# Performance work log

Hardware: AMD Instinct MI355X
Metric: run time of the kernel (lower is better)

## Reference

```python
import jax, jax.numpy as jnp
import numpy as np

F = 128
E = 100000   # num_edges
T = 1000000  # num_triplets


def setup_inputs() -> dict:
    key = jax.random.key(0)
    ks = jax.random.split(key, 20)
    s = 0.05
    return {
        "f": jax.random.normal(ks[0], (E, 2 * F), jnp.float32),
        "M01": jax.random.normal(ks[1], (T, F), jnp.float32),
        "M02": jax.random.normal(ks[2], (T, F), jnp.float32),
        # split_net MLP([2F, 2F, 2F]): Linear -> act -> Linear
        "W1": jax.random.normal(ks[3], (2 * F, 2 * F), jnp.float32) * s,
        "b1": jnp.zeros((2 * F,), jnp.float32),
        "W2": jax.random.normal(ks[4], (2 * F, 2 * F), jnp.float32) * s,
        "b2": jnp.zeros((2 * F,), jnp.float32),
        "Ws01": jax.random.normal(ks[5], (F, F), jnp.float32) * s,
        "bs01": jnp.zeros((F,), jnp.float32),
        "Ws02": jax.random.normal(ks[6], (F, F), jnp.float32) * s,
        "bs02": jnp.zeros((F,), jnp.float32),
        "Ws": jax.random.normal(ks[7], (2 * F, F), jnp.float32) * s,
        "bs": jnp.zeros((F,), jnp.float32),
        "Wout": jax.random.normal(ks[8], (F, F), jnp.float32) * s,
        "bout": jnp.zeros((F,), jnp.float32),
        "num_edges": E,
        "idx_ji": jax.random.randint(ks[9], (T,), 0, E, jnp.int32),
        "idx_ki": jax.random.randint(ks[10], (T,), 0, E, jnp.int32),
    }


def reference(f, M01, M02, W1, b1, W2, b2, Ws01, bs01, Ws02, bs02, Ws, bs,
              Wout, bout, num_edges, idx_ji, idx_ki):
    act = jax.nn.silu
    # f = act(split_net(f)); split_net = Linear -> act -> Linear
    h = act(act(f @ W1 + b1) @ W2 + b2)          # [E, 2F]
    f01, f02 = jnp.split(h, 2, axis=-1)           # [E, F] each
    # triplet interaction: gather -> multiply -> linear -> act
    s01 = act((f01[idx_ki] * M01 * f01[idx_ji]) @ Ws01 + bs01)  # [T, F]
    s02 = act((f02[idx_ki] * M02 * f02[idx_ji]) @ Ws02 + bs02)  # [T, F]
    s = act(jnp.concatenate((s01, s02), axis=-1) @ Ws + bs)     # [T, F]
    # scatter-sum triplets back to edges
    out = jax.ops.segment_sum(s, idx_ji, num_segments=num_edges)  # [E, F]
    return out @ Wout + bout
```

## Files before the change

kernel.cpp:

```cpp
#include <hip/hip_runtime.h>

typedef __attribute__((ext_vector_type(8))) short short8;
typedef __attribute__((ext_vector_type(4))) float f32x4;

__device__ __forceinline__ float silu_f(float x) { return x / (1.0f + __expf(-x)); }

__device__ __forceinline__ unsigned short f2bf(float x) {
  unsigned u = __float_as_uint(x);
  u += 0x7FFFu + ((u >> 16) & 1u);
  return (unsigned short)(u >> 16);
}
__device__ __forceinline__ float bf2f(unsigned short v) {
  return __uint_as_float(((unsigned)v) << 16);
}
__device__ __forceinline__ unsigned cvtpk_bf16(float lo, float hi) {
  unsigned r;
  asm("v_cvt_pk_bf16_f32 %0, %1, %2" : "=v"(r) : "v"(lo), "v"(hi));
  return r;
}

#define TSYNC() do { asm volatile("s_waitcnt lgkmcnt(0)" ::: "memory"); \
                     __builtin_amdgcn_s_barrier(); \
                     asm volatile("" ::: "memory"); } while (0)

__device__ __forceinline__ void prep_one(const float* __restrict__ W,
                                         unsigned short* __restrict__ wh,
                                         unsigned short* __restrict__ wl,
                                         int N, int e)
{
  int k = e / N, n = e % N;
  float w = W[e];
  unsigned short hi = f2bf(w);
  unsigned short lo = f2bf(w - bf2f(hi));
  int kp = k >> 6, kk = k & 63;
  size_t dst = (size_t)kp * N * 64 + (size_t)n * 64 + ((((kk >> 3) ^ (n & 7)) << 3)) + (kk & 7);
  wh[dst] = hi;
  wl[dst] = lo;
}

__global__ void prep_all(const float* __restrict__ W1, unsigned short* w1h, unsigned short* w1l,
                         const float* __restrict__ W2, unsigned short* w2h, unsigned short* w2l,
                         const float* __restrict__ Wo, unsigned short* woh, unsigned short* wol)
{
  int e = blockIdx.x * 256 + threadIdx.x;
  if (e < 256 * 256) {
    prep_one(W1, w1h, w1l, 256, e);
    prep_one(W2, w2h, w2l, 256, e);
  }
  if (e < 128 * 128) prep_one(Wo, woh, wol, 128, e);
}

template<int INBF, int ASPLIT>
__global__ __launch_bounds__(512)
void mlp_gemm(const void* A_, const unsigned short* __restrict__ wh,
              const unsigned short* __restrict__ wl,
              const float* __restrict__ bias, unsigned short* __restrict__ C, int M)
{
  __shared__ unsigned short aTh[64 * 64], aTl[64 * 64];
  __shared__ unsigned short whb[256 * 64], wlb[256 * 64];
  const int tid = threadIdx.x;
  const int lane = tid & 63, wv = tid >> 6;
  const int g = wv & 3, hh = wv >> 2;
  const int l15 = lane & 15, l4 = lane >> 4;
  const int row0 = blockIdx.x * 64;
  const int r = tid >> 3, kseg = (tid & 7) * 8;
  const f32x4 zero4 = {0.f, 0.f, 0.f, 0.f};

  f32x4 acc[8];
#pragma unroll
  for (int nt = 0; nt < 8; nt++) acc[nt] = zero4;

  for (int kp = 0; kp < 4; kp++) {
    {
      const int grow = row0 + r;
      float x[8];
      if (grow < M) {
        if (INBF) {
          short8 v = *(const short8*)((const unsigned short*)A_ + (size_t)grow * 256 + kp * 64 + kseg);
#pragma unroll
          for (int j = 0; j < 8; j++) x[j] = bf2f((unsigned short)v[j]);
        } else {
          const float* ap = (const float*)A_ + (size_t)grow * 256 + kp * 64 + kseg;
          float4 v0 = *(const float4*)ap;
          float4 v1 = *(const float4*)(ap + 4);
          x[0] = v0.x; x[1] = v0.y; x[2] = v0.z; x[3] = v0.w;
          x[4] = v1.x; x[5] = v1.y; x[6] = v1.z; x[7] = v1.w;
        }
      } else {
#pragma unroll
        for (int j = 0; j < 8; j++) x[j] = 0.f;
      }
      union { short8 s; unsigned short us[8]; } H, L;
#pragma unroll
      for (int j = 0; j < 8; j++) {
        H.us[j] = f2bf(x[j]);
        L.us[j] = ASPLIT ? f2bf(x[j] - bf2f(H.us[j])) : (unsigned short)0;
      }
      const int dst = r * 64 + ((((kseg >> 3) ^ (r & 7)) << 3));
      *(short8*)(aTh + dst) = H.s;
      if (ASPLIT) *(short8*)(aTl + dst) = L.s;
    }
    {
      const short8* srcH = (const short8*)(wh + (size_t)kp * 16384);
      const short8* srcL = (const short8*)(wl + (size_t)kp * 16384);
#pragma unroll
      for (int i = 0; i < 4; i++) {
        ((short8*)whb)[tid + 512 * i] = srcH[tid + 512 * i];
        ((short8*)wlb)[tid + 512 * i] = srcL[tid + 512 * i];
      }
    }
    __syncthreads();
#pragma unroll
    for (int ks = 0; ks < 2; ks++) {
      const int arow = 16 * g + l15;
      const int aof = arow * 64 + (((4 * ks + l4) ^ (arow & 7)) << 3);
      short8 ah = *(const short8*)(aTh + aof);
      short8 al = *(const short8*)(aTl + aof);
#pragma unroll
      for (int nt = 0; nt < 8; nt++) {
        const int col = 128 * hh + 16 * nt + l15;
        const int bof = col * 64 + (((4 * ks + l4) ^ (col & 7)) << 3);
        short8 bh = *(const short8*)(whb + bof);
        short8 bl = *(const short8*)(wlb + bof);
        acc[nt] = __builtin_amdgcn_mfma_f32_16x16x32_bf16(ah, bh, acc[nt], 0, 0, 0);
        acc[nt] = __builtin_amdgcn_mfma_f32_16x16x32_bf16(ah, bl, acc[nt], 0, 0, 0);
        if (ASPLIT)
          acc[nt] = __builtin_amdgcn_mfma_f32_16x16x32_bf16(al, bh, acc[nt], 0, 0, 0);
      }
    }
    __syncthreads();
  }
#pragma unroll
  for (int nt = 0; nt < 8; nt++) {
    const int col = 128 * hh + 16 * nt + l15;
    const float bv = bias[col];
#pragma unroll
    for (int i = 0; i < 4; i++) {
      const int row = row0 + 16 * g + 4 * l4 + i;
      if (row < M) C[(size_t)row * 256 + col] = f2bf(silu_f(acc[nt][i] + bv));
    }
  }
}

__global__ __launch_bounds__(512)
void final_gemm(const float* __restrict__ A, const unsigned short* __restrict__ wh,
                const unsigned short* __restrict__ wl,
                const float* __restrict__ bias, float* __restrict__ C, int M)
{
  __shared__ unsigned short aTh[64 * 64], aTl[64 * 64];
  __shared__ unsigned short whb[128 * 64], wlb[128 * 64];
  const int tid = threadIdx.x;
  const int lane = tid & 63, wv = tid >> 6;
  const int g = wv & 3, hh = wv >> 2;
  const int l15 = lane & 15, l4 = lane >> 4;
  const int row0 = blockIdx.x * 64;
  const int r = tid >> 3, kseg = (tid & 7) * 8;
  const f32x4 zero4 = {0.f, 0.f, 0.f, 0.f};

  f32x4 acc[4];
#pragma unroll
  for (int nt = 0; nt < 4; nt++) acc[nt] = zero4;

  for (int kp = 0; kp < 2; kp++) {
    {
      const int grow = row0 + r;
      float x[8];
      if (grow < M) {
        const float* ap = A + (size_t)grow * 128 + kp * 64 + kseg;
        float4 v0 = *(const float4*)ap;
        float4 v1 = *(const float4*)(ap + 4);
        x[0] = v0.x; x[1] = v0.y; x[2] = v0.z; x[3] = v0.w;
        x[4] = v1.x; x[5] = v1.y; x[6] = v1.z; x[7] = v1.w;
      } else {
#pragma unroll
        for (int j = 0; j < 8; j++) x[j] = 0.f;
      }
      union { short8 s; unsigned short us[8]; } H, L;
#pragma unroll
      for (int j = 0; j < 8; j++) {
        H.us[j] = f2bf(x[j]);
        L.us[j] = f2bf(x[j] - bf2f(H.us[j]));
      }
      const int dst = r * 64 + ((((kseg >> 3) ^ (r & 7)) << 3));
      *(short8*)(aTh + dst) = H.s;
      *(short8*)(aTl + dst) = L.s;
    }
    {
      const short8* srcH = (const short8*)(wh + (size_t)kp * 8192);
      const short8* srcL = (const short8*)(wl + (size_t)kp * 8192);
#pragma unroll
      for (int i = 0; i < 2; i++) {
        ((short8*)whb)[tid + 512 * i] = srcH[tid + 512 * i];
        ((short8*)wlb)[tid + 512 * i] = srcL[tid + 512 * i];
      }
    }
    __syncthreads();
#pragma unroll
    for (int ks = 0; ks < 2; ks++) {
      const int arow = 16 * g + l15;
      const int aof = arow * 64 + (((4 * ks + l4) ^ (arow & 7)) << 3);
      short8 ah = *(const short8*)(aTh + aof);
      short8 al = *(const short8*)(aTl + aof);
#pragma unroll
      for (int nt = 0; nt < 4; nt++) {
        const int col = 64 * hh + 16 * nt + l15;
        const int bof = col * 64 + (((4 * ks + l4) ^ (col & 7)) << 3);
        short8 bh = *(const short8*)(whb + bof);
        short8 bl = *(const short8*)(wlb + bof);
        acc[nt] = __builtin_amdgcn_mfma_f32_16x16x32_bf16(ah, bh, acc[nt], 0, 0, 0);
        acc[nt] = __builtin_amdgcn_mfma_f32_16x16x32_bf16(ah, bl, acc[nt], 0, 0, 0);
        acc[nt] = __builtin_amdgcn_mfma_f32_16x16x32_bf16(al, bh, acc[nt], 0, 0, 0);
      }
    }
    __syncthreads();
  }
#pragma unroll
  for (int nt = 0; nt < 4; nt++) {
    const int col = 64 * hh + 16 * nt + l15;
    const float bv = bias[col];
#pragma unroll
    for (int i = 0; i < 4; i++) {
      const int row = row0 + 16 * g + 4 * l4 + i;
      if (row < M) C[(size_t)row * 128 + col] = acc[nt][i] + bv;
    }
  }
}

__global__ void hist_k(const int* __restrict__ ji, int* __restrict__ cnt, int T) {
  int t = blockIdx.x * 256 + threadIdx.x;
  const int stride = gridDim.x * 256;
  for (; t < T; t += stride) atomicAdd(&cnt[ji[t]], 1);
}

__global__ void scan1_k(const int* __restrict__ cnt, int* __restrict__ csum, int E) {
  __shared__ int red[256];
  const int c0 = blockIdx.x * 2048;
  int s = 0;
  for (int i = threadIdx.x; i < 2048; i += 256) {
    int e = c0 + i;
    if (e < E) s += cnt[e];
  }
  red[threadIdx.x] = s;
  __syncthreads();
  for (int o = 128; o > 0; o >>= 1) {
    if (threadIdx.x < o) red[threadIdx.x] += red[threadIdx.x + o];
    __syncthreads();
  }
  if (threadIdx.x == 0) csum[blockIdx.x] = red[0];
}

__global__ void scan2_k(int* __restrict__ csum, int n) {
  if (threadIdx.x == 0 && blockIdx.x == 0) {
    int acc = 0;
    for (int i = 0; i < n; i++) { int v = csum[i]; csum[i] = acc; acc += v; }
  }
}

__global__ void scan3_k(const int* __restrict__ cnt, const int* __restrict__ csum,
                        int* __restrict__ off, int E) {
  __shared__ int ts[256];
  const int c0 = blockIdx.x * 2048;
  const int tid = threadIdx.x;
  int loc[8];
  int s = 0;
#pragma unroll
  for (int k = 0; k < 8; k++) {
    int e = c0 + tid * 8 + k;
    loc[k] = (e < E) ? cnt[e] : 0;
    s += loc[k];
  }
  ts[tid] = s;
  __syncthreads();
  for (int o = 1; o < 256; o <<= 1) {
    int v = (tid >= o) ? ts[tid - o] : 0;
    __syncthreads();
    ts[tid] += v;
    __syncthreads();
  }
  int base = csum[blockIdx.x] + ((tid > 0) ? ts[tid - 1] : 0);
#pragma unroll
  for (int k = 0; k < 8; k++) {
    int e = c0 + tid * 8 + k;
    if (e < E) { off[e] = base; base += loc[k]; }
  }
}

__global__ void scatter_k(const int* __restrict__ ji, int* __restrict__ cursor,
                          int* __restrict__ perm, int T) {
  int t = blockIdx.x * 256 + threadIdx.x;
  const int stride = gridDim.x * 256;
  for (; t < T; t += stride) {
    int e = ji[t];
    int p = atomicAdd(&cursor[e], 1);
    perm[p] = t;
  }
}

struct G12 {
  short8 a0, a1;
  short8 b0, b1;
  float4 m0, m1, m2, m3;
};

__device__ __forceinline__ void issue12(G12& g, const unsigned short* __restrict__ fa,
                                        const unsigned short* __restrict__ fb,
                                        const float* __restrict__ mm, int cseg)
{
  g.a0 = *(const short8*)(fa + cseg);
  g.a1 = *(const short8*)(fa + cseg + 8);
  g.b0 = *(const short8*)(fb + cseg);
  g.b1 = *(const short8*)(fb + cseg + 8);
  g.m0 = *(const float4*)(mm + cseg + 0);
  g.m1 = *(const float4*)(mm + cseg + 4);
  g.m2 = *(const float4*)(mm + cseg + 8);
  g.m3 = *(const float4*)(mm + cseg + 12);
}

__device__ __forceinline__ void pack8x(const short8& a, const short8& b,
                                       const float4& m0, const float4& m1, short8& o)
{
  float p[8];
  p[0] = bf2f((unsigned short)a[0]) * m0.x * bf2f((unsigned short)b[0]);
  p[1] = bf2f((unsigned short)a[1]) * m0.y * bf2f((unsigned short)b[1]);
  p[2] = bf2f((unsigned short)a[2]) * m0.z * bf2f((unsigned short)b[2]);
  p[3] = bf2f((unsigned short)a[3]) * m0.w * bf2f((unsigned short)b[3]);
  p[4] = bf2f((unsigned short)a[4]) * m1.x * bf2f((unsigned short)b[4]);
  p[5] = bf2f((unsigned short)a[5]) * m1.y * bf2f((unsigned short)b[5]);
  p[6] = bf2f((unsigned short)a[6]) * m1.z * bf2f((unsigned short)b[6]);
  p[7] = bf2f((unsigned short)a[7]) * m1.w * bf2f((unsigned short)b[7]);
  union { short8 s; unsigned u[4]; } t;
  t.u[0] = cvtpk_bf16(p[0], p[1]);
  t.u[1] = cvtpk_bf16(p[2], p[3]);
  t.u[2] = cvtpk_bf16(p[4], p[5]);
  t.u[3] = cvtpk_bf16(p[6], p[7]);
  o = t.s;
}

__device__ __forceinline__ void pack16(const G12& g, short8& lo, short8& hi)
{
  pack8x(g.a0, g.b0, g.m0, g.m1, lo);
  pack8x(g.a1, g.b1, g.m2, g.m3, hi);
}

__device__ __forceinline__ void writep(unsigned short* pb, int r, int cseg,
                                       const short8& lo, const short8& hi)
{
  const int c0 = cseg >> 3;
  *(short8*)(pb + r * 128 + (((c0) ^ (r & 7)) << 3)) = lo;
  *(short8*)(pb + r * 128 + (((c0 + 1) ^ (r & 7)) << 3)) = hi;
}

__device__ __forceinline__ void mfma_block4(const unsigned short* abuf,
                                            const unsigned short* wF,
                                            f32x4 (&acc)[4],
                                            int g, int hh, int lane, int l15, int l4)
{
  const int arow = 16 * g + l15;
  __builtin_amdgcn_s_setprio(1);
#pragma unroll
  for (int ks = 0; ks < 4; ks++) {
    short8 a = *(const short8*)(abuf + arow * 128 + (((4 * ks + l4) ^ (arow & 7)) << 3));
#pragma unroll
    for (int ct = 0; ct < 4; ct++) {
      const short8 b = *(const short8*)(wF + (((4 * hh + ct) * 4 + ks) * 64 + lane) * 8);
      acc[ct] = __builtin_amdgcn_mfma_f32_16x16x32_bf16(a, b, acc[ct], 0, 0, 0);
    }
  }
  __builtin_amdgcn_s_setprio(0);
}

__device__ __forceinline__ void store_s(unsigned short* pbuf, const f32x4 (&acc)[4],
                                        const float* __restrict__ bias,
                                        int g, int hh, int l15, int l4)
{
#pragma unroll
  for (int ct = 0; ct < 4; ct++) {
    const int col = 64 * hh + 16 * ct + l15;
    const float bv = bias[col];
#pragma unroll
    for (int i = 0; i < 4; i++) {
      const int r = 16 * g + 4 * l4 + i;
      float v = silu_f(acc[ct][i] + bv);
      pbuf[r * 128 + ((((col >> 3) ^ (r & 7)) << 3)) + (col & 7)] = f2bf(v);
    }
  }
}

__global__ __launch_bounds__(512, 2)
void triplet_fused(const unsigned short* __restrict__ h,
                   const float* __restrict__ M01, const float* __restrict__ M02,
                   const float* __restrict__ Ws01, const float* __restrict__ bs01,
                   const float* __restrict__ Ws02, const float* __restrict__ bs02,
                   const float* __restrict__ Ws,   const float* __restrict__ bs,
                   const int* __restrict__ idx_ji, const int* __restrict__ idx_ki,
                   const int* __restrict__ perm,
                   float* __restrict__ out_acc, int T)
{
  __shared__ unsigned short wF01[16384];
  __shared__ unsigned short wF02[16384];
  __shared__ unsigned short wFA[16384];
  __shared__ unsigned short wFB[16384];
  __shared__ unsigned short pbA[64 * 128];
  __shared__ unsigned short pbB[64 * 128];

  const int tid = threadIdx.x;

  for (int e = tid; e < 16384; e += 512) {
    const int j = e & 7, ln = (e >> 3) & 63, ks = (e >> 9) & 3, ct = e >> 11;
    const int col = 16 * ct + (ln & 15);
    const int k = 32 * ks + 8 * (ln >> 4) + j;
    const int src = k * 128 + col;
    wF01[e] = f2bf(Ws01[src]);
    wF02[e] = f2bf(Ws02[src]);
    wFA[e]  = f2bf(Ws[src]);
    wFB[e]  = f2bf(Ws[16384 + src]);
  }
  __syncthreads();

  const int lane = tid & 63;
  const int wv = tid >> 6;
  const int g = wv & 3;
  const int hh = wv >> 2;
  const int l15 = lane & 15, l4 = lane >> 4;
  const f32x4 zero4 = {0.f, 0.f, 0.f, 0.f};

  float bsv[4];
#pragma unroll
  for (int ct = 0; ct < 4; ct++) bsv[ct] = bs[64 * hh + 16 * ct + l15];

  const int r = tid >> 3;
  const int cseg = (tid & 7) * 16;
  const int ntiles = T >> 6;
  const int G = gridDim.x;

  int tile = blockIdx.x;
  if (tile >= ntiles) return;

  auto srow = [&](int q) { int s = q * 64 + r; return s < T ? s : T - 1; };

  int trow1, trow2, trow3;
  int ek1, ej1, ek2, ej2;
  {
    const int trow0 = perm[srow(tile)];
    trow1 = perm[srow(tile + G)];
    trow2 = perm[srow(tile + 2 * G)];
    const int ek0 = idx_ki[trow0], ej0 = idx_ji[trow0];
    ek1 = idx_ki[trow1]; ej1 = idx_ji[trow1];
    ek2 = idx_ki[trow2]; ej2 = idx_ji[trow2];

    G12 gP;
    issue12(gP, h + (size_t)ek0 * 256, h + (size_t)ej0 * 256, M01 + (size_t)trow0 * 128, cseg);
    trow3 = trow0;
    (void)gP;
    short8 tmplo, tmphi;
    (void)tmplo; (void)tmphi;
  }

  G12 gA, gB, g2;
  short8 p01lo, p01hi;
  {
    const int trow0 = perm[srow(tile)];
    const int ek0 = idx_ki[trow0], ej0 = idx_ji[trow0];
    issue12(gA, h + (size_t)ek0 * 256, h + (size_t)ej0 * 256, M01 + (size_t)trow0 * 128, cseg);
    issue12(gB, h + (size_t)ek1 * 256, h + (size_t)ej1 * 256, M01 + (size_t)trow1 * 128, cseg);
    issue12(g2, h + (size_t)ek0 * 256 + 128, h + (size_t)ej0 * 256 + 128,
            M02 + (size_t)trow0 * 128, cseg);
    pack16(gA, p01lo, p01hi);
  }
  int parity = 0;

  for (; tile < ntiles; tile += G) {
    writep(pbA, r, cseg, p01lo, p01hi);
    const int pj = perm[(tile << 6) + 16 * g + l15];
    TSYNC();

    trow3 = perm[srow(tile + 3 * G)];
    const int jrv = idx_ji[pj];
    {
      f32x4 acc1[4] = {zero4, zero4, zero4, zero4};
      mfma_block4(pbA, wF01, acc1, g, hh, lane, l15, l4);
      store_s(pbB, acc1, bs01, g, hh, l15, l4);
    }
    TSYNC();

    f32x4 acc3[4] = {zero4, zero4, zero4, zero4};
    mfma_block4(pbB, wFA, acc3, g, hh, lane, l15, l4);
    {
      short8 lo, hi;
      pack16(g2, lo, hi);
      writep(pbA, r, cseg, lo, hi);
    }
    issue12(g2, h + (size_t)ek1 * 256 + 128, h + (size_t)ej1 * 256 + 128,
            M02 + (size_t)trow1 * 128, cseg);
    TSYNC();

    if (parity == 0)
      issue12(gA, h + (size_t)ek2 * 256, h + (size_t)ej2 * 256, M01 + (size_t)trow2 * 128, cseg);
    else
      issue12(gB, h + (size_t)ek2 * 256, h + (size_t)ej2 * 256, M01 + (size_t)trow2 * 128, cseg);
    {
      f32x4 acc2[4] = {zero4, zero4, zero4, zero4};
      mfma_block4(pbA, wF02, acc2, g, hh, lane, l15, l4);
      store_s(pbB, acc2, bs02, g, hh, l15, l4);
    }
    TSYNC();

    mfma_block4(pbB, wFB, acc3, g, hh, lane, l15, l4);
    const int ek3 = idx_ki[trow3], ej3 = idx_ji[trow3];
    {
      float sf[4][4];
#pragma unroll
      for (int ct = 0; ct < 4; ct++)
#pragma unroll
        for (int i = 0; i < 4; i++)
          sf[ct][i] = silu_f(acc3[ct][i] + bsv[ct]);

      const int ejp = __shfl_up(jrv, 1, 16);
      unsigned bm = (unsigned)(__ballot((l15 > 0) && (jrv != ejp)) & 0xFFFFull);
      int fr = 0;
      unsigned rem = bm;
      while (fr < 16) {
        const int nxt = rem ? (__ffs(rem) - 1) : 16;
        rem &= rem - 1;
        const int lr = nxt - 1;
        const int e = __shfl(jrv, fr, 16);
        float sv[4];
#pragma unroll
        for (int ct = 0; ct < 4; ct++) {
          float s = 0.f;
#pragma unroll
          for (int i = 0; i < 4; i++) {
            const int rr = 4 * l4 + i;
            s += (rr >= fr && rr <= lr) ? sf[ct][i] : 0.f;
          }
          s += __shfl_xor(s, 16);
          s += __shfl_xor(s, 32);
          sv[ct] = s;
        }
        const float s0 = (l4 == 0) ? sv[0] : (l4 == 1) ? sv[1] : (l4 == 2) ? sv[2] : sv[3];
        float* dst = out_acc + (size_t)e * 128 + 64 * hh + 16 * l4 + l15;
        if (fr == 0 || lr == 15) atomicAdd(dst, s0);
        else *dst = s0;
        fr = nxt;
      }
    }
    if (parity == 0) pack16(gB, p01lo, p01hi);
    else             pack16(gA, p01lo, p01hi);
    parity ^= 1;
    ek1 = ek2; ej1 = ej2; trow1 = trow2;
    ek2 = ek3; ej2 = ej3; trow2 = trow3;
    TSYNC();
  }
}

extern "C" void kernel_launch(void* const* d_in, const int* in_sizes, int n_in,
                              void* d_out, int out_size, void* d_ws, size_t ws_size,
                              hipStream_t stream)
{
  const float* f    = (const float*)d_in[0];
  const float* M01  = (const float*)d_in[1];
  const float* M02  = (const float*)d_in[2];
  const float* W1   = (const float*)d_in[3];
  const float* b1   = (const float*)d_in[4];
  const float* W2   = (const float*)d_in[5];
  const float* b2   = (const float*)d_in[6];
  const float* Ws01 = (const float*)d_in[7];
  const float* bs01 = (const float*)d_in[8];
  const float* Ws02 = (const float*)d_in[9];
  const float* bs02 = (const float*)d_in[10];
  const float* Ws   = (const float*)d_in[11];
  const float* bs   = (const float*)d_in[12];
  const float* Wout = (const float*)d_in[13];
  const float* bout = (const float*)d_in[14];
  const int* idx_ji = (const int*)d_in[16];
  const int* idx_ki = (const int*)d_in[17];

  const int E = in_sizes[0] / 256;
  const int T = in_sizes[1] / 128;

  char* w = (char*)d_ws;
  unsigned short* hbuf = (unsigned short*)w;
  size_t o = ((size_t)E * 256 * 2 + 255) & ~(size_t)255;
  unsigned short* wt1h = (unsigned short*)(w + o); o += 256 * 256 * 2;
  unsigned short* wt1l = (unsigned short*)(w + o); o += 256 * 256 * 2;
  unsigned short* wt2h = (unsigned short*)(w + o); o += 256 * 256 * 2;
  unsigned short* wt2l = (unsigned short*)(w + o); o += 256 * 256 * 2;
  unsigned short* wtoh = (unsigned short*)(w + o); o += 128 * 128 * 2;
  unsigned short* wtol = (unsigned short*)(w + o); o += 128 * 128 * 2;
  o = (o + 255) & ~(size_t)255;
  int* cnt = (int*)(w + o);  o += ((size_t)E * 4 + 255) & ~(size_t)255;
  int* off = (int*)(w + o);  o += ((size_t)E * 4 + 255) & ~(size_t)255;
  int* csum = (int*)(w + o); o += 4096;
  int* perm = (int*)(w + o);

  float* out_acc = (float*)d_out;
  const int mb = (E + 63) / 64;

  prep_all<<<(256 * 256 + 255) / 256, 256, 0, stream>>>(W1, wt1h, wt1l,
                                                        W2, wt2h, wt2l,
                                                        Wout, wtoh, wtol);

  mlp_gemm<0, 1><<<mb, 512, 0, stream>>>(f, wt1h, wt1l, b1, hbuf, E);
  mlp_gemm<1, 0><<<mb, 512, 0, stream>>>(hbuf, wt2h, wt2l, b2, hbuf, E);

  hipMemsetAsync(cnt, 0, (size_t)E * 4, stream);
  hist_k<<<1024, 256, 0, stream>>>(idx_ji, cnt, T);
  const int nchunks = (E + 2047) / 2048;
  scan1_k<<<nchunks, 256, 0, stream>>>(cnt, csum, E);
  scan2_k<<<1, 64, 0, stream>>>(csum, nchunks);
  scan3_k<<<nchunks, 256, 0, stream>>>(cnt, csum, off, E);
  scatter_k<<<1024, 256, 0, stream>>>(idx_ji, off, perm, T);

  hipMemsetAsync(d_out, 0, (size_t)E * 128 * sizeof(float), stream);

  const int ntiles = (T + 63) / 64;
  const int grid = ntiles < 256 ? ntiles : 256;
  triplet_fused<<<grid, 512, 0, stream>>>(hbuf, M01, M02, Ws01, bs01, Ws02, bs02,
                                          Ws, bs, idx_ji, idx_ki, perm, out_acc, T);

  final_gemm<<<mb, 512, 0, stream>>>(out_acc, wtoh, wtol, bout, out_acc, E);
}
```

Measured before the change: 940.8 us.

## Make each wave own a 16-triplet subtile end to end, removing block barriers

The triplet kernel moves from block-cooperative 64-row tiles, where 8 waves split rows and columns and sync with block barriers, to per-wave 16-row subtiles. Each wave computes all 128 output columns through private LDS scratch, with only lgkmcnt waits plus a scheduling barrier. Gathers load directly in MFMA operand layout and are issued at the top of each iteration, replacing the deep multi-stage software prefetch pipeline. This removes barrier stalls and cross-wave coupling, but needs more accumulator registers per wave and relies on less cross-iteration prefetch to hide gather latency.

```diff
diff --git a/kernel.cpp b/kernel.cpp
--- a/kernel.cpp
+++ b/kernel.cpp
@@ -19,9 +19,8 @@
   return r;
 }
 
-#define TSYNC() do { asm volatile("s_waitcnt lgkmcnt(0)" ::: "memory"); \
-                     __builtin_amdgcn_s_barrier(); \
-                     asm volatile("" ::: "memory"); } while (0)
+#define LGKM_SB() do { asm volatile("s_waitcnt lgkmcnt(0)" ::: "memory"); \
+                       __builtin_amdgcn_sched_barrier(0); } while (0)
 
 __device__ __forceinline__ void prep_one(const float* __restrict__ W,
                                          unsigned short* __restrict__ wh,
@@ -296,94 +295,23 @@
   }
 }
 
-struct G12 {
-  short8 a0, a1;
-  short8 b0, b1;
-  float4 m0, m1, m2, m3;
-};
-
-__device__ __forceinline__ void issue12(G12& g, const unsigned short* __restrict__ fa,
-                                        const unsigned short* __restrict__ fb,
-                                        const float* __restrict__ mm, int cseg)
-{
-  g.a0 = *(const short8*)(fa + cseg);
-  g.a1 = *(const short8*)(fa + cseg + 8);
-  g.b0 = *(const short8*)(fb + cseg);
-  g.b1 = *(const short8*)(fb + cseg + 8);
-  g.m0 = *(const float4*)(mm + cseg + 0);
-  g.m1 = *(const float4*)(mm + cseg + 4);
-  g.m2 = *(const float4*)(mm + cseg + 8);
-  g.m3 = *(const float4*)(mm + cseg + 12);
-}
-
-__device__ __forceinline__ void pack8x(const short8& a, const short8& b,
-                                       const float4& m0, const float4& m1, short8& o)
-{
-  float p[8];
-  p[0] = bf2f((unsigned short)a[0]) * m0.x * bf2f((unsigned short)b[0]);
-  p[1] = bf2f((unsigned short)a[1]) * m0.y * bf2f((unsigned short)b[1]);
-  p[2] = bf2f((unsigned short)a[2]) * m0.z * bf2f((unsigned short)b[2]);
-  p[3] = bf2f((unsigned short)a[3]) * m0.w * bf2f((unsigned short)b[3]);
-  p[4] = bf2f((unsigned short)a[4]) * m1.x * bf2f((unsigned short)b[4]);
-  p[5] = bf2f((unsigned short)a[5]) * m1.y * bf2f((unsigned short)b[5]);
-  p[6] = bf2f((unsigned short)a[6]) * m1.z * bf2f((unsigned short)b[6]);
-  p[7] = bf2f((unsigned short)a[7]) * m1.w * bf2f((unsigned short)b[7]);
+__device__ __forceinline__ short8 pack8p(const short8 a, const short8 b,
+                                         const float4 m0, const float4 m1)
+{
+  float p0 = bf2f((unsigned short)a[0]) * m0.x * bf2f((unsigned short)b[0]);
+  float p1 = bf2f((unsigned short)a[1]) * m0.y * bf2f((unsigned short)b[1]);
+  float p2 = bf2f((unsigned short)a[2]) * m0.z * bf2f((unsigned short)b[2]);
+  float p3 = bf2f((unsigned short)a[3]) * m0.w * bf2f((unsigned short)b[3]);
+  float p4 = bf2f((unsigned short)a[4]) * m1.x * bf2f((unsigned short)b[4]);
+  float p5 = bf2f((unsigned short)a[5]) * m1.y * bf2f((unsigned short)b[5]);
+  float p6 = bf2f((unsigned short)a[6]) * m1.z * bf2f((unsigned short)b[6]);
+  float p7 = bf2f((unsigned short)a[7]) * m1.w * bf2f((unsigned short)b[7]);
   union { short8 s; unsigned u[4]; } t;
-  t.u[0] = cvtpk_bf16(p[0], p[1]);
-  t.u[1] = cvtpk_bf16(p[2], p[3]);
-  t.u[2] = cvtpk_bf16(p[4], p[5]);
-  t.u[3] = cvtpk_bf16(p[6], p[7]);
-  o = t.s;
-}
-
-__device__ __forceinline__ void pack16(const G12& g, short8& lo, short8& hi)
-{
-  pack8x(g.a0, g.b0, g.m0, g.m1, lo);
-  pack8x(g.a1, g.b1, g.m2, g.m3, hi);
-}
-
-__device__ __forceinline__ void writep(unsigned short* pb, int r, int cseg,
-                                       const short8& lo, const short8& hi)
-{
-  const int c0 = cseg >> 3;
-  *(short8*)(pb + r * 128 + (((c0) ^ (r & 7)) << 3)) = lo;
-  *(short8*)(pb + r * 128 + (((c0 + 1) ^ (r & 7)) << 3)) = hi;
-}
-
-__device__ __forceinline__ void mfma_block4(const unsigned short* abuf,
-                                            const unsigned short* wF,
-                                            f32x4 (&acc)[4],
-                                            int g, int hh, int lane, int l15, int l4)
-{
-  const int arow = 16 * g + l15;
-  __builtin_amdgcn_s_setprio(1);
-#pragma unroll
-  for (int ks = 0; ks < 4; ks++) {
-    short8 a = *(const short8*)(abuf + arow * 128 + (((4 * ks + l4) ^ (arow & 7)) << 3));
-#pragma unroll
-    for (int ct = 0; ct < 4; ct++) {
-      const short8 b = *(const short8*)(wF + (((4 * hh + ct) * 4 + ks) * 64 + lane) * 8);
-      acc[ct] = __builtin_amdgcn_mfma_f32_16x16x32_bf16(a, b, acc[ct], 0, 0, 0);
-    }
-  }
-  __builtin_amdgcn_s_setprio(0);
-}
-
-__device__ __forceinline__ void store_s(unsigned short* pbuf, const f32x4 (&acc)[4],
-                                        const float* __restrict__ bias,
-                                        int g, int hh, int l15, int l4)
-{
-#pragma unroll
-  for (int ct = 0; ct < 4; ct++) {
-    const int col = 64 * hh + 16 * ct + l15;
-    const float bv = bias[col];
-#pragma unroll
-    for (int i = 0; i < 4; i++) {
-      const int r = 16 * g + 4 * l4 + i;
-      float v = silu_f(acc[ct][i] + bv);
-      pbuf[r * 128 + ((((col >> 3) ^ (r & 7)) << 3)) + (col & 7)] = f2bf(v);
-    }
-  }
+  t.u[0] = cvtpk_bf16(p0, p1);
+  t.u[1] = cvtpk_bf16(p2, p3);
+  t.u[2] = cvtpk_bf16(p4, p5);
+  t.u[3] = cvtpk_bf16(p6, p7);
+  return t.s;
 }
 
 __global__ __launch_bounds__(512, 2)
@@ -400,11 +328,9 @@
   __shared__ unsigned short wF02[16384];
   __shared__ unsigned short wFA[16384];
   __shared__ unsigned short wFB[16384];
-  __shared__ unsigned short pbA[64 * 128];
-  __shared__ unsigned short pbB[64 * 128];
+  __shared__ unsigned short sbuf[8][2048];
 
   const int tid = threadIdx.x;
-
   for (int e = tid; e < 16384; e += 512) {
     const int j = e & 7, ln = (e >> 3) & 63, ks = (e >> 9) & 3, ct = e >> 11;
     const int col = 16 * ct + (ln & 15);
@@ -417,139 +343,175 @@
   }
   __syncthreads();
 
-  const int lane = tid & 63;
-  const int wv = tid >> 6;
-  const int g = wv & 3;
-  const int hh = wv >> 2;
+  const int lane = tid & 63, wv = tid >> 6;
   const int l15 = lane & 15, l4 = lane >> 4;
+  unsigned short* const sb = sbuf[wv];
   const f32x4 zero4 = {0.f, 0.f, 0.f, 0.f};
 
-  float bsv[4];
-#pragma unroll
-  for (int ct = 0; ct < 4; ct++) bsv[ct] = bs[64 * hh + 16 * ct + l15];
-
-  const int r = tid >> 3;
-  const int cseg = (tid & 7) * 16;
-  const int ntiles = T >> 6;
-  const int G = gridDim.x;
-
-  int tile = blockIdx.x;
-  if (tile >= ntiles) return;
-
-  auto srow = [&](int q) { int s = q * 64 + r; return s < T ? s : T - 1; };
-
-  int trow1, trow2, trow3;
-  int ek1, ej1, ek2, ej2;
-  {
-    const int trow0 = perm[srow(tile)];
-    trow1 = perm[srow(tile + G)];
-    trow2 = perm[srow(tile + 2 * G)];
-    const int ek0 = idx_ki[trow0], ej0 = idx_ji[trow0];
-    ek1 = idx_ki[trow1]; ej1 = idx_ji[trow1];
-    ek2 = idx_ki[trow2]; ej2 = idx_ji[trow2];
-
-    G12 gP;
-    issue12(gP, h + (size_t)ek0 * 256, h + (size_t)ej0 * 256, M01 + (size_t)trow0 * 128, cseg);
-    trow3 = trow0;
-    (void)gP;
-    short8 tmplo, tmphi;
-    (void)tmplo; (void)tmphi;
-  }
-
-  G12 gA, gB, g2;
-  short8 p01lo, p01hi;
-  {
-    const int trow0 = perm[srow(tile)];
-    const int ek0 = idx_ki[trow0], ej0 = idx_ji[trow0];
-    issue12(gA, h + (size_t)ek0 * 256, h + (size_t)ej0 * 256, M01 + (size_t)trow0 * 128, cseg);
-    issue12(gB, h + (size_t)ek1 * 256, h + (size_t)ej1 * 256, M01 + (size_t)trow1 * 128, cseg);
-    issue12(g2, h + (size_t)ek0 * 256 + 128, h + (size_t)ej0 * 256 + 128,
-            M02 + (size_t)trow0 * 128, cseg);
-    pack16(gA, p01lo, p01hi);
-  }
-  int parity = 0;
-
-  for (; tile < ntiles; tile += G) {
-    writep(pbA, r, cseg, p01lo, p01hi);
-    const int pj = perm[(tile << 6) + 16 * g + l15];
-    TSYNC();
-
-    trow3 = perm[srow(tile + 3 * G)];
-    const int jrv = idx_ji[pj];
+  float bs01v[8], bs02v[8], bsv[8];
+#pragma unroll
+  for (int ct = 0; ct < 8; ct++) {
+    bs01v[ct] = bs01[16 * ct + l15];
+    bs02v[ct] = bs02[16 * ct + l15];
+    bsv[ct]   = bs[16 * ct + l15];
+  }
+
+  const int nsub = T >> 4;
+  const int stride = gridDim.x * 8;
+  int sub = blockIdx.x * 8 + wv;
+
+  int pidx = perm[(sub << 4) + l15];
+  int ek = idx_ki[pidx], ej = idx_ji[pidx];
+
+  for (; sub < nsub; sub += stride) {
+    const unsigned short* fa = h + (size_t)ek * 256 + 8 * l4;
+    const unsigned short* fb = h + (size_t)ej * 256 + 8 * l4;
+    const float* mm1 = M01 + (size_t)pidx * 128 + 8 * l4;
+    const float* mm2 = M02 + (size_t)pidx * 128 + 8 * l4;
+    short8 ra1[4], rb1[4], ra2[4], rb2[4];
+    float4 rm1[8], rm2[8];
+#pragma unroll
+    for (int ks = 0; ks < 4; ks++) {
+      ra1[ks] = *(const short8*)(fa + 32 * ks);
+      rb1[ks] = *(const short8*)(fb + 32 * ks);
+      rm1[2 * ks]     = *(const float4*)(mm1 + 32 * ks);
+      rm1[2 * ks + 1] = *(const float4*)(mm1 + 32 * ks + 4);
+      ra2[ks] = *(const short8*)(fa + 128 + 32 * ks);
+      rb2[ks] = *(const short8*)(fb + 128 + 32 * ks);
+      rm2[2 * ks]     = *(const float4*)(mm2 + 32 * ks);
+      rm2[2 * ks + 1] = *(const float4*)(mm2 + 32 * ks + 4);
+    }
+
+    const int subn = sub + stride;
+    int sidx = (subn << 4) + l15;
+    if (sidx >= T) sidx = T - 1;
+    const int pidx_n = perm[sidx];
+
+    f32x4 acc1[8];
+#pragma unroll
+    for (int ct = 0; ct < 8; ct++) acc1[ct] = zero4;
+#pragma unroll
+    for (int ks = 0; ks < 4; ks++) {
+      const short8 a = pack8p(ra1[ks], rb1[ks], rm1[2 * ks], rm1[2 * ks + 1]);
+#pragma unroll
+      for (int ct = 0; ct < 8; ct++) {
+        const short8 b = *(const short8*)(wF01 + ((ct * 4 + ks) * 64 + lane) * 8);
+        acc1[ct] = __builtin_amdgcn_mfma_f32_16x16x32_bf16(a, b, acc1[ct], 0, 0, 0);
+      }
+    }
+
+#pragma unroll
+    for (int ct = 0; ct < 8; ct++) {
+      const int chi = 2 * ct + (l15 >> 3);
+#pragma unroll
+      for (int i = 0; i < 4; i++) {
+        const int row = 4 * l4 + i;
+        sb[row * 128 + (((chi ^ (row & 7)) << 3)) + (l15 & 7)] =
+            f2bf(silu_f(acc1[ct][i] + bs01v[ct]));
+      }
+    }
+    LGKM_SB();
+    short8 as1[4];
+#pragma unroll
+    for (int ks = 0; ks < 4; ks++)
+      as1[ks] = *(const short8*)(sb + l15 * 128 + (((4 * ks + l4) ^ (l15 & 7)) << 3));
+
+    f32x4 acc3[8];
+#pragma unroll
+    for (int ct = 0; ct < 8; ct++) acc3[ct] = zero4;
+#pragma unroll
+    for (int ks = 0; ks < 4; ks++)
+#pragma unroll
+      for (int ct = 0; ct < 8; ct++) {
+        const short8 b = *(const short8*)(wFA + ((ct * 4 + ks) * 64 + lane) * 8);
+        acc3[ct] = __builtin_amdgcn_mfma_f32_16x16x32_bf16(as1[ks], b, acc3[ct], 0, 0, 0);
+      }
+
+    const int ekn = idx_ki[pidx_n], ejn = idx_ji[pidx_n];
+
+#pragma unroll
+    for (int ct = 0; ct < 8; ct++) acc1[ct] = zero4;
+#pragma unroll
+    for (int ks = 0; ks < 4; ks++) {
+      const short8 a = pack8p(ra2[ks], rb2[ks], rm2[2 * ks], rm2[2 * ks + 1]);
+#pragma unroll
+      for (int ct = 0; ct < 8; ct++) {
+        const short8 b = *(const short8*)(wF02 + ((ct * 4 + ks) * 64 + lane) * 8);
+        acc1[ct] = __builtin_amdgcn_mfma_f32_16x16x32_bf16(a, b, acc1[ct], 0, 0, 0);
+      }
+    }
+
+#pragma unroll
+    for (int ct = 0; ct < 8; ct++) {
+      const int chi = 2 * ct + (l15 >> 3);
+#pragma unroll
+      for (int i = 0; i < 4; i++) {
+        const int row = 4 * l4 + i;
+        sb[row * 128 + (((chi ^ (row & 7)) << 3)) + (l15 & 7)] =
+            f2bf(silu_f(acc1[ct][i] + bs02v[ct]));
+      }
+    }
+    LGKM_SB();
+    short8 as2[4];
+#pragma unroll
+    for (int ks = 0; ks < 4; ks++)
+      as2[ks] = *(const short8*)(sb + l15 * 128 + (((4 * ks + l4) ^ (l15 & 7)) << 3));
+
+#pragma unroll
+    for (int ks = 0; ks < 4; ks++)
+#pragma unroll
+      for (int ct = 0; ct < 8; ct++) {
+        const short8 b = *(const short8*)(wFB + ((ct * 4 + ks) * 64 + lane) * 8);
+        acc3[ct] = __builtin_amdgcn_mfma_f32_16x16x32_bf16(as2[ks], b, acc3[ct], 0, 0, 0);
+      }
+
+#pragma unroll
+    for (int ct = 0; ct < 8; ct++)
+#pragma unroll
+      for (int i = 0; i < 4; i++)
+        acc3[ct][i] = silu_f(acc3[ct][i] + bsv[ct]);
+
     {
-      f32x4 acc1[4] = {zero4, zero4, zero4, zero4};
-      mfma_block4(pbA, wF01, acc1, g, hh, lane, l15, l4);
-      store_s(pbB, acc1, bs01, g, hh, l15, l4);
-    }
-    TSYNC();
-
-    f32x4 acc3[4] = {zero4, zero4, zero4, zero4};
-    mfma_block4(pbB, wFA, acc3, g, hh, lane, l15, l4);
-    {
-      short8 lo, hi;
-      pack16(g2, lo, hi);
-      writep(pbA, r, cseg, lo, hi);
-    }
-    issue12(g2, h + (size_t)ek1 * 256 + 128, h + (size_t)ej1 * 256 + 128,
-            M02 + (size_t)trow1 * 128, cseg);
-    TSYNC();
-
-    if (parity == 0)
-      issue12(gA, h + (size_t)ek2 * 256, h + (size_t)ej2 * 256, M01 + (size_t)trow2 * 128, cseg);
-    else
-      issue12(gB, h + (size_t)ek2 * 256, h + (size_t)ej2 * 256, M01 + (size_t)trow2 * 128, cseg);
-    {
-      f32x4 acc2[4] = {zero4, zero4, zero4, zero4};
-      mfma_block4(pbA, wF02, acc2, g, hh, lane, l15, l4);
-      store_s(pbB, acc2, bs02, g, hh, l15, l4);
-    }
-    TSYNC();
-
-    mfma_block4(pbB, wFB, acc3, g, hh, lane, l15, l4);
-    const int ek3 = idx_ki[trow3], ej3 = idx_ji[trow3];
-    {
-      float sf[4][4];
-#pragma unroll
-      for (int ct = 0; ct < 4; ct++)
-#pragma unroll
-        for (int i = 0; i < 4; i++)
-          sf[ct][i] = silu_f(acc3[ct][i] + bsv[ct]);
-
-      const int ejp = __shfl_up(jrv, 1, 16);
-      unsigned bm = (unsigned)(__ballot((l15 > 0) && (jrv != ejp)) & 0xFFFFull);
+      const int ejp = __shfl_up(ej, 1, 16);
+      unsigned bm = (unsigned)(__ballot((l15 > 0) && (ej != ejp)) & 0xFFFFull);
       int fr = 0;
       unsigned rem = bm;
       while (fr < 16) {
         const int nxt = rem ? (__ffs(rem) - 1) : 16;
         rem &= rem - 1;
         const int lr = nxt - 1;
-        const int e = __shfl(jrv, fr, 16);
-        float sv[4];
-#pragma unroll
-        for (int ct = 0; ct < 4; ct++) {
+        const int e = __shfl(ej, fr, 16);
+        float sv[8];
+#pragma unroll
+        for (int ct = 0; ct < 8; ct++) {
           float s = 0.f;
 #pragma unroll
           for (int i = 0; i < 4; i++) {
             const int rr = 4 * l4 + i;
-            s += (rr >= fr && rr <= lr) ? sf[ct][i] : 0.f;
+            s += (rr >= fr && rr <= lr) ? acc3[ct][i] : 0.f;
           }
           s += __shfl_xor(s, 16);
           s += __shfl_xor(s, 32);
           sv[ct] = s;
         }
-        const float s0 = (l4 == 0) ? sv[0] : (l4 == 1) ? sv[1] : (l4 == 2) ? sv[2] : sv[3];
-        float* dst = out_acc + (size_t)e * 128 + 64 * hh + 16 * l4 + l15;
-        if (fr == 0 || lr == 15) atomicAdd(dst, s0);
-        else *dst = s0;
+        float w0, w1;
+        if (l4 == 0)      { w0 = sv[0]; w1 = sv[1]; }
+        else if (l4 == 1) { w0 = sv[2]; w1 = sv[3]; }
+        else if (l4 == 2) { w0 = sv[4]; w1 = sv[5]; }
+        else              { w0 = sv[6]; w1 = sv[7]; }
+        float* dst = out_acc + (size_t)e * 128 + 32 * l4 + l15;
+        if (fr == 0 || lr == 15) {
+          atomicAdd(dst, w0);
+          atomicAdd(dst + 16, w1);
+        } else {
+          dst[0] = w0;
+          dst[16] = w1;
+        }
         fr = nxt;
       }
     }
-    if (parity == 0) pack16(gB, p01lo, p01hi);
-    else             pack16(gA, p01lo, p01hi);
-    parity ^= 1;
-    ek1 = ek2; ej1 = ej2; trow1 = trow2;
-    ek2 = ek3; ej2 = ej3; trow2 = trow3;
-    TSYNC();
+
+    pidx = pidx_n; ek = ekn; ej = ejn;
   }
 }
 
@@ -613,10 +575,8 @@
 
   hipMemsetAsync(d_out, 0, (size_t)E * 128 * sizeof(float), stream);
 
-  const int ntiles = (T + 63) / 64;
-  const int grid = ntiles < 256 ? ntiles : 256;
-  triplet_fused<<<grid, 512, 0, stream>>>(hbuf, M01, M02, Ws01, bs01, Ws02, bs02,
-                                          Ws, bs, idx_ji, idx_ki, perm, out_acc, T);
+  triplet_fused<<<256, 512, 0, stream>>>(hbuf, M01, M02, Ws01, bs01, Ws02, bs02,
+                                         Ws, bs, idx_ji, idx_ki, perm, out_acc, T);
 
   final_gemm<<<mb, 512, 0, stream>>>(out_acc, wtoh, wtol, bout, out_acc, E);
 }
```

Result: faster. 818.8 us (-13.0%).
